# Optimization experiments

Hardware: AMD Instinct MI355X
Metric: run time of the kernel (lower is better)

## Reference

```python
import jax, jax.numpy as jnp
import numpy as np

B, C, H, W = 16, 384, 32, 32
NUM_HEADS = 8
HEAD_DIM = C // NUM_HEADS
SCALE = HEAD_DIM ** -0.5


def setup_inputs() -> dict:
    key = jax.random.key(0)
    k0, k1, k2, k3 = jax.random.split(key, 4)
    s = 0.02
    return {
        "x": jax.random.normal(k0, (B, C, H, W), dtype=jnp.float32),
        "w_qkv": jax.random.normal(k1, (3 * C, C), dtype=jnp.float32) * s,  # torch Linear weight [out,in]
        "w_proj": jax.random.normal(k2, (C, C), dtype=jnp.float32) * s,
        "b_proj": jax.random.normal(k3, (C,), dtype=jnp.float32) * s,
    }


def reference(x, w_qkv, w_proj, b_proj):
    b, c, h, w = x.shape
    n = h * w
    # flatten(2).transpose(1,2): (B,C,H,W) -> (B,N,C)
    xt = x.reshape(b, c, n).transpose(0, 2, 1)
    # qkv linear (no bias): (B,N,3C)
    qkv = jnp.einsum("bnc,oc->bno", xt, w_qkv)
    qkv = qkv.reshape(b, n, 3, NUM_HEADS, HEAD_DIM).transpose(2, 0, 3, 1, 4)
    q, k, v = qkv[0], qkv[1], qkv[2]  # each (B, heads, N, hd)
    attn = jnp.einsum("bhnd,bhmd->bhnm", q, k) * SCALE
    attn = jax.nn.softmax(attn, axis=-1)
    out = jnp.einsum("bhnm,bhmd->bhnd", attn, v)  # (B, heads, N, hd)
    out = out.transpose(0, 2, 1, 3).reshape(b, n, c)  # (B,N,C)
    out = jnp.einsum("bnc,oc->bno", out, w_proj) + b_proj
    # rearrange b (h w) c -> b c h w
    return out.transpose(0, 2, 1).reshape(b, c, h, w)
```

## Files before the change

kernel.cpp:

```cpp
#include <hip/hip_runtime.h>
#include <hip/hip_bf16.h>
#include <math.h>

constexpr int Bn     = 16;
constexpr int Cc     = 384;
constexpr int Nn     = 1024;
constexpr int NHEADS = 8;
constexpr int HD     = 48;
constexpr float SCALE = 0.14433756729740643f;
constexpr float SCL2  = 0.14433756729740643f * 1.4426950408889634f;

using bf16x8 = __attribute__((ext_vector_type(8))) short;
using bf16x4 = __attribute__((ext_vector_type(4))) short;
using f32x4  = __attribute__((ext_vector_type(4))) float;

__device__ inline short f2b(float f) {
    __hip_bfloat16 h = __float2bfloat16(f);
    return *reinterpret_cast<short*>(&h);
}

__device__ __forceinline__ void gload16(const short* g, short* l) {
    __builtin_amdgcn_global_load_lds(
        (const __attribute__((address_space(1))) void*)(g),
        (__attribute__((address_space(3))) void*)(l),
        16, 0, 0);
}

__global__ __launch_bounds__(256) void conv_cast2(const float* __restrict__ in1,
                                                  short* __restrict__ hi1, int n1,
                                                  const float* __restrict__ in2,
                                                  short* __restrict__ hi2, int n2)
{
    int u = blockIdx.x * 256 + threadIdx.x;
    const float* in; short* hi; int i;
    if (u * 4 < n1) { in = in1; hi = hi1; i = u * 4; }
    else {
        i = u * 4 - n1;
        if (i >= n2) return;
        in = in2; hi = hi2;
    }
    float4 v = *reinterpret_cast<const float4*>(&in[i]);
    bf16x4 h = { f2b(v.x), f2b(v.y), f2b(v.z), f2b(v.w) };
    *reinterpret_cast<bf16x4*>(&hi[i]) = h;
}

__global__ __launch_bounds__(256) void prep_xt(const float* __restrict__ x,
                                               short* __restrict__ xt)
{
    const int b  = blockIdx.z;
    const int c0 = blockIdx.y * 64;
    const int n0 = blockIdx.x * 64;
    __shared__ float T[64 * 68];

    const int tid = threadIdx.x;
    const int r   = tid >> 2;
    const int seg = tid & 3;

    const float* xb = x + ((size_t)b * Cc + c0) * Nn;
#pragma unroll
    for (int i = 0; i < 4; ++i) {
        float4 v = *reinterpret_cast<const float4*>(&xb[(size_t)r * Nn + n0 + seg * 16 + i * 4]);
        *reinterpret_cast<float4*>(&T[r * 68 + seg * 16 + i * 4]) = v;
    }
    __syncthreads();

    short* oh = xt + ((size_t)b * Nn + n0 + r) * Cc + c0;
#pragma unroll
    for (int i = 0; i < 4; ++i) {
        bf16x4 hv;
#pragma unroll
        for (int j = 0; j < 4; ++j)
            hv[j] = f2b(T[(seg * 16 + i * 4 + j) * 68 + r]);
        *reinterpret_cast<bf16x4*>(&oh[seg * 16 + i * 4]) = hv;
    }
}

template <int MODE>
__global__ __launch_bounds__(256) void gemm_bf16(const short* __restrict__ Whi,
                                                 const short* __restrict__ Xh,
                                                 short* __restrict__ Yqk,
                                                 short* __restrict__ Yv,
                                                 float* __restrict__ Yf,
                                                 const float* __restrict__ bias,
                                                 int M, int K, int NN)
{
    const int b  = blockIdx.z;
    const int m0 = blockIdx.y * 128;
    const int n0 = blockIdx.x * 128;
    const short* Xb = Xh + (size_t)b * NN * K;

    constexpr int BUFS = 8192;
    constexpr int OA = 0;
    constexpr int OB = 4096;
    __shared__ __align__(16) short smem[17408];

    const int tid  = threadIdx.x;
    const int lane = tid & 63;
    const int wave = tid >> 6;
    const int c    = lane & 15;
    const int h4   = lane >> 4;
    const int wr   = wave >> 1;
    const int wc   = wave & 1;

    const int sq   = ((tid & 3) ^ ((tid >> 3) & 3)) * 8;
    const int lds0 = wave * 512;
    const int lds1 = 2048 + wave * 512;

    const short* gW = Whi + (size_t)(m0 + (tid >> 2)) * K + sq;
    const short* gX = Xb + (size_t)(n0 + (tid >> 2)) * K + sq;
    const size_t rowskip = (size_t)64 * K;

    const int sw = (h4 ^ ((c >> 1) & 3)) * 8;

    f32x4 acc[4][4];
#pragma unroll
    for (int mi = 0; mi < 4; ++mi)
#pragma unroll
        for (int ni = 0; ni < 4; ++ni) acc[mi][ni] = 0.0f;

    gload16(gW,           smem + OA + lds0);
    gload16(gW + rowskip, smem + OA + lds1);
    gload16(gX,           smem + OB + lds0);
    gload16(gX + rowskip, smem + OB + lds1);
    __syncthreads();

    const int NT = K >> 5;
    for (int t = 0; t < NT; ++t) {
        short* cbuf = smem + (t & 1) * BUFS;

        if (t + 1 < NT) {
            short* nbuf = smem + ((t + 1) & 1) * BUFS;
            const int nk = (t + 1) * 32;
            gload16(gW + nk,           nbuf + OA + lds0);
            gload16(gW + rowskip + nk, nbuf + OA + lds1);
            gload16(gX + nk,           nbuf + OB + lds0);
            gload16(gX + rowskip + nk, nbuf + OB + lds1);
        }

        bf16x8 a[4], bb[4];
#pragma unroll
        for (int mi = 0; mi < 4; ++mi) {
            int row = wr * 64 + mi * 16 + c;
            a[mi] = *reinterpret_cast<const bf16x8*>(&cbuf[OA + row * 32 + sw]);
        }
#pragma unroll
        for (int ni = 0; ni < 4; ++ni) {
            int row = wc * 64 + ni * 16 + c;
            bb[ni] = *reinterpret_cast<const bf16x8*>(&cbuf[OB + row * 32 + sw]);
        }
        __builtin_amdgcn_s_setprio(1);
#pragma unroll
        for (int mi = 0; mi < 4; ++mi)
#pragma unroll
            for (int ni = 0; ni < 4; ++ni)
                acc[mi][ni] = __builtin_amdgcn_mfma_f32_16x16x32_bf16(a[mi], bb[ni], acc[mi][ni], 0, 0, 0);
        __builtin_amdgcn_s_setprio(0);

        __syncthreads();
    }

    if (MODE == 0) {
        if (m0 < 768) {
            const float qscale = (m0 < 384) ? SCL2 : 1.0f;
            short* Cs = smem;
#pragma unroll
            for (int mi = 0; mi < 4; ++mi)
#pragma unroll
                for (int ni = 0; ni < 4; ++ni) {
                    int nl = wc * 64 + ni * 16 + c;
                    int cl = wr * 64 + mi * 16 + 4 * h4;
                    bf16x4 pk;
#pragma unroll
                    for (int r = 0; r < 4; ++r) pk[r] = f2b(acc[mi][ni][r] * qscale);
                    *reinterpret_cast<bf16x4*>(&Cs[nl * 136 + cl]) = pk;
                }
            __syncthreads();
#pragma unroll
            for (int l = 0; l < 8; ++l) {
                int u  = tid + l * 256;
                int nl = u >> 4, ch = u & 15;
                *reinterpret_cast<bf16x8*>(&Yqk[((size_t)b * NN + n0 + nl) * 768 + m0 + ch * 8]) =
                    *reinterpret_cast<const bf16x8*>(&Cs[nl * 136 + ch * 8]);
            }
        } else {
            short* Cs = smem;
#pragma unroll
            for (int mi = 0; mi < 4; ++mi)
#pragma unroll
                for (int ni = 0; ni < 4; ++ni) {
                    int npb = wc * 64 + 32 * (ni >> 1) + 8 * (c >> 2) + 4 * (ni & 1) + (c & 3);
#pragma unroll
                    for (int r = 0; r < 4; ++r) {
                        int ml = wr * 64 + mi * 16 + h4 * 4 + r;
                        Cs[ml * 136 + npb] = f2b(acc[mi][ni][r]);
                    }
                }
            __syncthreads();
            short* Yb = Yv + (size_t)b * Cc * NN;
            const int srow2 = tid >> 1;
            const int cseg  = (tid & 1) * 64;
#pragma unroll
            for (int i = 0; i < 8; ++i)
                *reinterpret_cast<bf16x8*>(&Yb[(size_t)(m0 - 768 + srow2) * NN + n0 + cseg + i * 8]) =
                    *reinterpret_cast<const bf16x8*>(&Cs[srow2 * 136 + cseg + i * 8]);
        }
    } else {
        float* Yb = Yf + (size_t)b * M * NN;
        float* Cf = reinterpret_cast<float*>(smem);
        const int mr2 = tid >> 2;
        const int seg = tid & 3;
#pragma unroll
        for (int half = 0; half < 2; ++half) {
            __syncthreads();
            if (wr == half) {
#pragma unroll
                for (int mi = 0; mi < 4; ++mi)
#pragma unroll
                    for (int ni = 0; ni < 4; ++ni)
#pragma unroll
                        for (int r = 0; r < 4; ++r) {
                            int ml = mi * 16 + h4 * 4 + r;
                            int nl = wc * 64 + ni * 16 + c;
                            Cf[ml * 132 + nl] = acc[mi][ni][r];
                        }
            }
            __syncthreads();
            float bv = bias ? bias[m0 + half * 64 + mr2] : 0.0f;
#pragma unroll
            for (int i = 0; i < 8; ++i) {
                float4 v = *reinterpret_cast<const float4*>(&Cf[mr2 * 132 + seg * 32 + i * 4]);
                v.x += bv; v.y += bv; v.z += bv; v.w += bv;
                *reinterpret_cast<float4*>(&Yb[(size_t)(m0 + half * 64 + mr2) * NN + n0 + seg * 32 + i * 4]) = v;
            }
        }
    }
}

__global__ __launch_bounds__(256, 4) void attn_mfma(const short* __restrict__ qk_t,
                                                    const short* __restrict__ v_cn,
                                                    short* __restrict__ aot)
{
    const int id = blockIdx.x;
    const int rx = id & 7;
    const int kk = id >> 3;
    const int bh = rx * 16 + (kk & 15);
    const int qt = kk >> 4;
    const int b  = bh >> 3;
    const int h  = bh & 7;
    const int n0 = qt * 128;

    __shared__ __align__(16) short smem[16384];

    const int tid  = threadIdx.x;
    const int lane = tid & 63;
    const int wave = tid >> 6;
    const int c    = lane & 15;
    const int h4   = lane >> 4;
    const int qb   = n0 + wave * 32;

    const short* Qb    = qk_t + ((size_t)b * Nn + qb) * 768 + h * HD;
    const short* Kbase = qk_t + (size_t)b * Nn * 768 + 384 + h * HD;
    const short* Vb    = v_cn + ((size_t)b * Cc + h * HD) * Nn;

    const bf16x8 z8 = {};

    {
        int i0 = tid * 4;
        short v = (i0 < 64) ? (short)0x3F80 : (short)0;
        bf16x4 iv = {v, v, v, v};
        *reinterpret_cast<bf16x4*>(&smem[4096 + 3072 + i0]) = iv;
        *reinterpret_cast<bf16x4*>(&smem[12288 + 3072 + i0]) = iv;
    }

    bf16x8 qf0[2], qf1[2];
#pragma unroll
    for (int s = 0; s < 2; ++s) {
        const short* qrow = Qb + (size_t)(s * 16 + c) * 768;
        qf0[s] = *reinterpret_cast<const bf16x8*>(qrow + 8 * h4);
        qf1[s] = (h4 < 2) ? *reinterpret_cast<const bf16x8*>(qrow + 32 + 8 * h4) : z8;
    }

    const int u0 = wave * 64 + lane;
    const int r0 = u0 >> 3;
    const int sc0 = ((u0 & 7) ^ (r0 & 7)) * 8;
    const int u1 = 256 + u0;
    const int r1 = u1 >> 3;
    const int sc1 = ((u1 & 7) ^ (r1 & 7)) * 8;

    const int cs8 = c & 7;
    const int ks0 = (h4 ^ cs8) * 8;
    const int ks1 = ((4 + h4) ^ cs8) * 8;

    f32x4 o[2][3];
#pragma unroll
    for (int s = 0; s < 2; ++s)
#pragma unroll
        for (int jd = 0; jd < 3; ++jd) o[s][jd] = 0.0f;
    f32x4 o3[2];
    o3[0] = 0.0f; o3[1] = 0.0f;

    {
        short* Ksb = smem;
        short* Vsb = smem + 4096;
        gload16(Kbase + (size_t)r0 * 768 + sc0, Ksb + wave * 512);
        gload16(Kbase + (size_t)r1 * 768 + sc1, Ksb + 2048 + wave * 512);
        gload16(Vb + (size_t)r0 * Nn + sc0, Vsb + wave * 512);
        if (wave < 2)
            gload16(Vb + (size_t)r1 * Nn + sc1, Vsb + 2048 + wave * 512);
    }
    __syncthreads();

    for (int t = 0; t < 16; ++t) {
        const short* Ks = smem + (t & 1) * 8192;
        const short* Vs = Ks + 4096;

        if (t + 1 < 16) {
            short* Ksn = smem + ((t + 1) & 1) * 8192;
            short* Vsn = Ksn + 4096;
            const int mn = (t + 1) * 64;
            gload16(Kbase + (size_t)(mn + r0) * 768 + sc0, Ksn + wave * 512);
            gload16(Kbase + (size_t)(mn + r1) * 768 + sc1, Ksn + 2048 + wave * 512);
            gload16(Vb + (size_t)r0 * Nn + mn + sc0, Vsn + wave * 512);
            if (wave < 2)
                gload16(Vb + (size_t)r1 * Nn + mn + sc1, Vsn + 2048 + wave * 512);
        }

        f32x4 s4a[4], s4b[4];
#pragma unroll
        for (int j = 0; j < 4; ++j) { s4a[j] = 0.0f; s4b[j] = 0.0f; }
        __builtin_amdgcn_s_setprio(1);
#pragma unroll
        for (int j = 0; j < 4; ++j) {
            int kr = (16 * j + c) * 64;
            bf16x8 kc0 = *reinterpret_cast<const bf16x8*>(&Ks[kr + ks0]);
            bf16x8 kc1 = *reinterpret_cast<const bf16x8*>(&Ks[kr + ks1]);
            s4a[j] = __builtin_amdgcn_mfma_f32_16x16x32_bf16(kc0, qf0[0], s4a[j], 0, 0, 0);
            s4a[j] = __builtin_amdgcn_mfma_f32_16x16x32_bf16(kc1, qf1[0], s4a[j], 0, 0, 0);
            s4b[j] = __builtin_amdgcn_mfma_f32_16x16x32_bf16(kc0, qf0[1], s4b[j], 0, 0, 0);
            s4b[j] = __builtin_amdgcn_mfma_f32_16x16x32_bf16(kc1, qf1[1], s4b[j], 0, 0, 0);
        }
        __builtin_amdgcn_s_setprio(0);

        bf16x8 pa[2][2];
        {
            float p[4][4];
#pragma unroll
            for (int j = 0; j < 4; ++j)
#pragma unroll
                for (int r = 0; r < 4; ++r)
                    p[j][r] = exp2f(s4a[j][r]);
#pragma unroll
            for (int r = 0; r < 4; ++r) {
                pa[0][0][r]     = f2b(p[0][r]);
                pa[0][0][4 + r] = f2b(p[1][r]);
                pa[0][1][r]     = f2b(p[2][r]);
                pa[0][1][4 + r] = f2b(p[3][r]);
            }
        }
        {
            float p[4][4];
#pragma unroll
            for (int j = 0; j < 4; ++j)
#pragma unroll
                for (int r = 0; r < 4; ++r)
                    p[j][r] = exp2f(s4b[j][r]);
#pragma unroll
            for (int r = 0; r < 4; ++r) {
                pa[1][0][r]     = f2b(p[0][r]);
                pa[1][0][4 + r] = f2b(p[1][r]);
                pa[1][1][r]     = f2b(p[2][r]);
                pa[1][1][4 + r] = f2b(p[3][r]);
            }
        }

        __builtin_amdgcn_s_setprio(1);
#pragma unroll
        for (int jd = 0; jd < 4; ++jd) {
            int vr = (16 * jd + c) * 64;
            bf16x8 vf0 = *reinterpret_cast<const bf16x8*>(&Vs[vr + ks0]);
            bf16x8 vf1 = *reinterpret_cast<const bf16x8*>(&Vs[vr + ks1]);
            if (jd < 3) {
                o[0][jd] = __builtin_amdgcn_mfma_f32_16x16x32_bf16(vf0, pa[0][0], o[0][jd], 0, 0, 0);
                o[0][jd] = __builtin_amdgcn_mfma_f32_16x16x32_bf16(vf1, pa[0][1], o[0][jd], 0, 0, 0);
                o[1][jd] = __builtin_amdgcn_mfma_f32_16x16x32_bf16(vf0, pa[1][0], o[1][jd], 0, 0, 0);
                o[1][jd] = __builtin_amdgcn_mfma_f32_16x16x32_bf16(vf1, pa[1][1], o[1][jd], 0, 0, 0);
            } else {
                o3[0] = __builtin_amdgcn_mfma_f32_16x16x32_bf16(vf0, pa[0][0], o3[0], 0, 0, 0);
                o3[0] = __builtin_amdgcn_mfma_f32_16x16x32_bf16(vf1, pa[0][1], o3[0], 0, 0, 0);
                o3[1] = __builtin_amdgcn_mfma_f32_16x16x32_bf16(vf0, pa[1][0], o3[1], 0, 0, 0);
                o3[1] = __builtin_amdgcn_mfma_f32_16x16x32_bf16(vf1, pa[1][1], o3[1], 0, 0, 0);
            }
        }
        __builtin_amdgcn_s_setprio(0);

        __syncthreads();
    }

#pragma unroll
    for (int set = 0; set < 2; ++set) {
        float ls = __shfl(o3[set][0], c);
        float linv = 1.0f / ls;
        size_t rowoff = ((size_t)b * Nn + qb + set * 16 + c) * Cc + h * HD;
#pragma unroll
        for (int jd = 0; jd < 3; ++jd) {
            bf16x4 hv;
#pragma unroll
            for (int r = 0; r < 4; ++r)
                hv[r] = f2b(o[set][jd][r] * linv);
            *reinterpret_cast<bf16x4*>(&aot[rowoff + 16 * jd + 4 * h4]) = hv;
        }
    }
}

extern "C" void kernel_launch(void* const* d_in, const int* in_sizes, int n_in,
                              void* d_out, int out_size, void* d_ws, size_t ws_size,
                              hipStream_t stream)
{
    const float* x      = (const float*)d_in[0];
    const float* w_qkv  = (const float*)d_in[1];
    const float* w_proj = (const float*)d_in[2];
    const float* b_proj = (const float*)d_in[3];
    float* out = (float*)d_out;

    short* ws = (short*)d_ws;
    const size_t XT = (size_t)Bn * Nn * Cc;
    short* xt    = ws;
    short* wq_hi = xt + XT;
    short* wp_hi = wq_hi + (size_t)3 * Cc * Cc;
    short* qk_t  = wp_hi + (size_t)Cc * Cc;
    short* v_cn  = qk_t + (size_t)Bn * Nn * 768;
    short* aot   = v_cn + XT;

    {
        int n1 = 3 * Cc * Cc, n2 = Cc * Cc;
        int units = (n1 + n2) / 4;
        conv_cast2<<<(units + 255) / 256, 256, 0, stream>>>(
            w_qkv, wq_hi, n1, w_proj, wp_hi, n2);
    }
    prep_xt<<<dim3(Nn / 64, Cc / 64, Bn), 256, 0, stream>>>(x, xt);

    gemm_bf16<0><<<dim3(Nn / 128, (3 * Cc) / 128, Bn), 256, 0, stream>>>(
        wq_hi, xt, qk_t, v_cn, nullptr, nullptr, 3 * Cc, Cc, Nn);

    attn_mfma<<<1024, 256, 0, stream>>>(qk_t, v_cn, aot);

    gemm_bf16<1><<<dim3(Nn / 128, Cc / 128, Bn), 256, 0, stream>>>(
        wp_hi, aot, nullptr, nullptr, out, b_proj, Cc, Cc, Nn);
}
```

Baseline: 112.8 us.

## Double queries per attention wave to 64 for greater K/V tile reuse

Each attention block now covers 256 queries instead of 128, with each wave handling four 16-row query sets rather than two. Every K/V tile staged in shared memory is reused across twice as many query rows, and the grid is halved to 512 blocks. This cuts K/V load traffic and synchronisation per query. In exchange it roughly doubles accumulator and score registers, lowers the occupancy hint to 2 blocks, and leaves fewer blocks to spread across CUs.

Result: no change. 111.5 us (-1.2%).

```diff
diff --git a/kernel.cpp b/kernel.cpp
--- a/kernel.cpp
+++ b/kernel.cpp
@@ -236,7 +236,7 @@
     }
 }
 
-__global__ __launch_bounds__(256, 4) void attn_mfma(const short* __restrict__ qk_t,
+__global__ __launch_bounds__(256, 2) void attn_mfma(const short* __restrict__ qk_t,
                                                     const short* __restrict__ v_cn,
                                                     short* __restrict__ aot)
 {
@@ -247,7 +247,7 @@
     const int qt = kk >> 4;
     const int b  = bh >> 3;
     const int h  = bh & 7;
-    const int n0 = qt * 128;
+    const int n0 = qt * 256;
 
     __shared__ __align__(16) short smem[16384];
 
@@ -256,7 +256,7 @@
     const int wave = tid >> 6;
     const int c    = lane & 15;
     const int h4   = lane >> 4;
-    const int qb   = n0 + wave * 32;
+    const int qb   = n0 + wave * 64;
 
     const short* Qb    = qk_t + ((size_t)b * Nn + qb) * 768 + h * HD;
     const short* Kbase = qk_t + (size_t)b * Nn * 768 + 384 + h * HD;
@@ -272,9 +272,9 @@
         *reinterpret_cast<bf16x4*>(&smem[12288 + 3072 + i0]) = iv;
     }
 
-    bf16x8 qf0[2], qf1[2];
-#pragma unroll
-    for (int s = 0; s < 2; ++s) {
+    bf16x8 qf0[4], qf1[4];
+#pragma unroll
+    for (int s = 0; s < 4; ++s) {
         const short* qrow = Qb + (size_t)(s * 16 + c) * 768;
         qf0[s] = *reinterpret_cast<const bf16x8*>(qrow + 8 * h4);
         qf1[s] = (h4 < 2) ? *reinterpret_cast<const bf16x8*>(qrow + 32 + 8 * h4) : z8;
@@ -291,13 +291,14 @@
     const int ks0 = (h4 ^ cs8) * 8;
     const int ks1 = ((4 + h4) ^ cs8) * 8;
 
-    f32x4 o[2][3];
-#pragma unroll
-    for (int s = 0; s < 2; ++s)
+    f32x4 o[4][3];
+#pragma unroll
+    for (int s = 0; s < 4; ++s)
 #pragma unroll
         for (int jd = 0; jd < 3; ++jd) o[s][jd] = 0.0f;
-    f32x4 o3[2];
-    o3[0] = 0.0f; o3[1] = 0.0f;
+    f32x4 o3[4];
+#pragma unroll
+    for (int s = 0; s < 4; ++s) o3[s] = 0.0f;
 
     {
         short* Ksb = smem;
@@ -325,51 +326,40 @@
                 gload16(Vb + (size_t)r1 * Nn + mn + sc1, Vsn + 2048 + wave * 512);
         }
 
-        f32x4 s4a[4], s4b[4];
-#pragma unroll
-        for (int j = 0; j < 4; ++j) { s4a[j] = 0.0f; s4b[j] = 0.0f; }
+        f32x4 s4[4][4];
+#pragma unroll
+        for (int s = 0; s < 4; ++s)
+#pragma unroll
+            for (int j = 0; j < 4; ++j) s4[s][j] = 0.0f;
         __builtin_amdgcn_s_setprio(1);
 #pragma unroll
         for (int j = 0; j < 4; ++j) {
             int kr = (16 * j + c) * 64;
             bf16x8 kc0 = *reinterpret_cast<const bf16x8*>(&Ks[kr + ks0]);
             bf16x8 kc1 = *reinterpret_cast<const bf16x8*>(&Ks[kr + ks1]);
-            s4a[j] = __builtin_amdgcn_mfma_f32_16x16x32_bf16(kc0, qf0[0], s4a[j], 0, 0, 0);
-            s4a[j] = __builtin_amdgcn_mfma_f32_16x16x32_bf16(kc1, qf1[0], s4a[j], 0, 0, 0);
-            s4b[j] = __builtin_amdgcn_mfma_f32_16x16x32_bf16(kc0, qf0[1], s4b[j], 0, 0, 0);
-            s4b[j] = __builtin_amdgcn_mfma_f32_16x16x32_bf16(kc1, qf1[1], s4b[j], 0, 0, 0);
+#pragma unroll
+            for (int s = 0; s < 4; ++s) {
+                s4[s][j] = __builtin_amdgcn_mfma_f32_16x16x32_bf16(kc0, qf0[s], s4[s][j], 0, 0, 0);
+                s4[s][j] = __builtin_amdgcn_mfma_f32_16x16x32_bf16(kc1, qf1[s], s4[s][j], 0, 0, 0);
+            }
         }
         __builtin_amdgcn_s_setprio(0);
 
-        bf16x8 pa[2][2];
-        {
+        bf16x8 pa[4][2];
+#pragma unroll
+        for (int s = 0; s < 4; ++s) {
             float p[4][4];
 #pragma unroll
             for (int j = 0; j < 4; ++j)
 #pragma unroll
                 for (int r = 0; r < 4; ++r)
-                    p[j][r] = exp2f(s4a[j][r]);
+                    p[j][r] = exp2f(s4[s][j][r]);
 #pragma unroll
             for (int r = 0; r < 4; ++r) {
-                pa[0][0][r]     = f2b(p[0][r]);
-                pa[0][0][4 + r] = f2b(p[1][r]);
-                pa[0][1][r]     = f2b(p[2][r]);
-                pa[0][1][4 + r] = f2b(p[3][r]);
-            }
-        }
-        {
-            float p[4][4];
-#pragma unroll
-            for (int j = 0; j < 4; ++j)
-#pragma unroll
-                for (int r = 0; r < 4; ++r)
-                    p[j][r] = exp2f(s4b[j][r]);
-#pragma unroll
-            for (int r = 0; r < 4; ++r) {
-                pa[1][0][r]     = f2b(p[0][r]);
-                pa[1][0][4 + r] = f2b(p[1][r]);
-                pa[1][1][r]     = f2b(p[2][r]);
-                pa[1][1][4 + r] = f2b(p[3][r]);
+                pa[s][0][r]     = f2b(p[0][r]);
+                pa[s][0][4 + r] = f2b(p[1][r]);
+                pa[s][1][r]     = f2b(p[2][r]);
+                pa[s][1][4 + r] = f2b(p[3][r]);
             }
         }
 
@@ -380,15 +370,17 @@
             bf16x8 vf0 = *reinterpret_cast<const bf16x8*>(&Vs[vr + ks0]);
             bf16x8 vf1 = *reinterpret_cast<const bf16x8*>(&Vs[vr + ks1]);
             if (jd < 3) {
-                o[0][jd] = __builtin_amdgcn_mfma_f32_16x16x32_bf16(vf0, pa[0][0], o[0][jd], 0, 0, 0);
-                o[0][jd] = __builtin_amdgcn_mfma_f32_16x16x32_bf16(vf1, pa[0][1], o[0][jd], 0, 0, 0);
-                o[1][jd] = __builtin_amdgcn_mfma_f32_16x16x32_bf16(vf0, pa[1][0], o[1][jd], 0, 0, 0);
-                o[1][jd] = __builtin_amdgcn_mfma_f32_16x16x32_bf16(vf1, pa[1][1], o[1][jd], 0, 0, 0);
+#pragma unroll
+                for (int s = 0; s < 4; ++s) {
+                    o[s][jd] = __builtin_amdgcn_mfma_f32_16x16x32_bf16(vf0, pa[s][0], o[s][jd], 0, 0, 0);
+                    o[s][jd] = __builtin_amdgcn_mfma_f32_16x16x32_bf16(vf1, pa[s][1], o[s][jd], 0, 0, 0);
+                }
             } else {
-                o3[0] = __builtin_amdgcn_mfma_f32_16x16x32_bf16(vf0, pa[0][0], o3[0], 0, 0, 0);
-                o3[0] = __builtin_amdgcn_mfma_f32_16x16x32_bf16(vf1, pa[0][1], o3[0], 0, 0, 0);
-                o3[1] = __builtin_amdgcn_mfma_f32_16x16x32_bf16(vf0, pa[1][0], o3[1], 0, 0, 0);
-                o3[1] = __builtin_amdgcn_mfma_f32_16x16x32_bf16(vf1, pa[1][1], o3[1], 0, 0, 0);
+#pragma unroll
+                for (int s = 0; s < 4; ++s) {
+                    o3[s] = __builtin_amdgcn_mfma_f32_16x16x32_bf16(vf0, pa[s][0], o3[s], 0, 0, 0);
+                    o3[s] = __builtin_amdgcn_mfma_f32_16x16x32_bf16(vf1, pa[s][1], o3[s], 0, 0, 0);
+                }
             }
         }
         __builtin_amdgcn_s_setprio(0);
@@ -397,7 +389,7 @@
     }
 
 #pragma unroll
-    for (int set = 0; set < 2; ++set) {
+    for (int set = 0; set < 4; ++set) {
         float ls = __shfl(o3[set][0], c);
         float linv = 1.0f / ls;
         size_t rowoff = ((size_t)b * Nn + qb + set * 16 + c) * Cc + h * HD;
@@ -442,7 +434,7 @@
     gemm_bf16<0><<<dim3(Nn / 128, (3 * Cc) / 128, Bn), 256, 0, stream>>>(
         wq_hi, xt, qk_t, v_cn, nullptr, nullptr, 3 * Cc, Cc, Nn);
 
-    attn_mfma<<<1024, 256, 0, stream>>>(qk_t, v_cn, aot);
+    attn_mfma<<<512, 256, 0, stream>>>(qk_t, v_cn, aot);
 
     gemm_bf16<1><<<dim3(Nn / 128, Cc / 128, Bn), 256, 0, stream>>>(
         wp_hi, aot, nullptr, nullptr, out, b_proj, Cc, Cc, Nn);
```

## Triple-buffer K/V tiles in attention with two-deep prefetch and explicit vmcnt waits

Applied to the files above, without the earlier changes.

Moves the attention kernel's K/V staging from double buffering to a three-buffer ring, so loads are issued two tiles ahead. The block-wide __syncthreads is replaced by partial s_waitcnt vmcnt counts plus raw barriers. The V second-half load now runs on all four waves, with duplicate writes from waves 2-3, instead of being guarded by wave<2. The aim is to hide global-to-LDS latency better, at the cost of 48KB of LDS per block and a lower launch-bounds occupancy hint of 3.

New measurement: 113.7 us. Within noise of the previous version (+0.8%).

```diff
diff --git a/kernel.cpp b/kernel.cpp
--- a/kernel.cpp
+++ b/kernel.cpp
@@ -236,7 +236,7 @@
     }
 }
 
-__global__ __launch_bounds__(256, 4) void attn_mfma(const short* __restrict__ qk_t,
+__global__ __launch_bounds__(256, 3) void attn_mfma(const short* __restrict__ qk_t,
                                                     const short* __restrict__ v_cn,
                                                     short* __restrict__ aot)
 {
@@ -249,7 +249,7 @@
     const int h  = bh & 7;
     const int n0 = qt * 128;
 
-    __shared__ __align__(16) short smem[16384];
+    __shared__ __align__(16) short smem[24576];
 
     const int tid  = threadIdx.x;
     const int lane = tid & 63;
@@ -268,8 +268,9 @@
         int i0 = tid * 4;
         short v = (i0 < 64) ? (short)0x3F80 : (short)0;
         bf16x4 iv = {v, v, v, v};
-        *reinterpret_cast<bf16x4*>(&smem[4096 + 3072 + i0]) = iv;
-        *reinterpret_cast<bf16x4*>(&smem[12288 + 3072 + i0]) = iv;
+        *reinterpret_cast<bf16x4*>(&smem[7168 + i0])  = iv;
+        *reinterpret_cast<bf16x4*>(&smem[15360 + i0]) = iv;
+        *reinterpret_cast<bf16x4*>(&smem[23552 + i0]) = iv;
     }
 
     bf16x8 qf0[2], qf1[2];
@@ -286,6 +287,10 @@
     const int u1 = 256 + u0;
     const int r1 = u1 >> 3;
     const int sc1 = ((u1 & 7) ^ (r1 & 7)) * 8;
+    const int u1v = 256 + (wave & 1) * 64 + lane;
+    const int r1v = u1v >> 3;
+    const int sc1v = ((u1v & 7) ^ (r1v & 7)) * 8;
+    const int vdst1 = 4096 + 2048 + (wave & 1) * 512;
 
     const int cs8 = c & 7;
     const int ks0 = (h4 ^ cs8) * 8;
@@ -299,31 +304,27 @@
     f32x4 o3[2];
     o3[0] = 0.0f; o3[1] = 0.0f;
 
-    {
-        short* Ksb = smem;
-        short* Vsb = smem + 4096;
-        gload16(Kbase + (size_t)r0 * 768 + sc0, Ksb + wave * 512);
-        gload16(Kbase + (size_t)r1 * 768 + sc1, Ksb + 2048 + wave * 512);
-        gload16(Vb + (size_t)r0 * Nn + sc0, Vsb + wave * 512);
-        if (wave < 2)
-            gload16(Vb + (size_t)r1 * Nn + sc1, Vsb + 2048 + wave * 512);
-    }
-    __syncthreads();
+#define STAGE(BUF, MT)                                                          \
+    gload16(Kbase + (size_t)((MT) + r0) * 768 + sc0, (BUF) + wave * 512);       \
+    gload16(Kbase + (size_t)((MT) + r1) * 768 + sc1, (BUF) + 2048 + wave * 512);\
+    gload16(Vb + (size_t)r0 * Nn + (MT) + sc0, (BUF) + 4096 + wave * 512);      \
+    gload16(Vb + (size_t)r1v * Nn + (MT) + sc1v, (BUF) + vdst1);
+
+    short* cur = smem;
+    short* nxt = smem + 8192;
+    short* fut = smem + 16384;
+
+    STAGE(cur, 0);
+    STAGE(nxt, 64);
+    asm volatile("s_waitcnt vmcnt(4) lgkmcnt(0)" ::: "memory");
+    __builtin_amdgcn_s_barrier();
+    __builtin_amdgcn_sched_barrier(0);
 
     for (int t = 0; t < 16; ++t) {
-        const short* Ks = smem + (t & 1) * 8192;
-        const short* Vs = Ks + 4096;
-
-        if (t + 1 < 16) {
-            short* Ksn = smem + ((t + 1) & 1) * 8192;
-            short* Vsn = Ksn + 4096;
-            const int mn = (t + 1) * 64;
-            gload16(Kbase + (size_t)(mn + r0) * 768 + sc0, Ksn + wave * 512);
-            gload16(Kbase + (size_t)(mn + r1) * 768 + sc1, Ksn + 2048 + wave * 512);
-            gload16(Vb + (size_t)r0 * Nn + mn + sc0, Vsn + wave * 512);
-            if (wave < 2)
-                gload16(Vb + (size_t)r1 * Nn + mn + sc1, Vsn + 2048 + wave * 512);
-        }
+        if (t + 2 < 16) { STAGE(fut, (t + 2) * 64); }
+
+        const short* Ks = cur;
+        const short* Vs = cur + 4096;
 
         f32x4 s4a[4], s4b[4];
 #pragma unroll
@@ -393,8 +394,14 @@
         }
         __builtin_amdgcn_s_setprio(0);
 
-        __syncthreads();
-    }
+        if (t + 2 < 16) asm volatile("s_waitcnt vmcnt(4)" ::: "memory");
+        else            asm volatile("s_waitcnt vmcnt(0)" ::: "memory");
+        __builtin_amdgcn_s_barrier();
+        __builtin_amdgcn_sched_barrier(0);
+
+        short* tmp = cur; cur = nxt; nxt = fut; fut = tmp;
+    }
+#undef STAGE
 
 #pragma unroll
     for (int set = 0; set < 2; ++set) {
```
